# Kernel tuning notes

Hardware: AMD Instinct MI355X
Metric: run time of the kernel (lower is better)

The kernel has to match this reference:

```python
import jax, jax.numpy as jnp
import numpy as np

B, NB, T, NC = 32, 55, 512, 8
D, H, E, K, DEPTH, FF = 128, 8, 8, 2, 4, 512  # embed, heads, experts, top_k, depth, ffn hidden=4*D
IN = NB * NC  # 440


def _ln(x, g, b, eps=1e-5):
    m = jnp.mean(x, axis=-1, keepdims=True)
    v = jnp.mean((x - m) ** 2, axis=-1, keepdims=True)
    return (x - m) / jnp.sqrt(v + eps) * g + b


def setup_inputs() -> dict:
    key = jax.random.key(0)
    ks = jax.random.split(key, 16)
    s = 0.02
    return {
        "x": jax.random.normal(ks[0], (B, NB, T, NC), jnp.float32),
        "proj_W": jax.random.normal(ks[1], (IN, D), jnp.float32) * s,
        "proj_b": jnp.zeros((D,), jnp.float32),
        "pos_embed": jax.random.normal(ks[2], (1, T, D), jnp.float32) * s,
        "ln1_g": jnp.ones((DEPTH, D), jnp.float32),
        "ln1_b": jnp.zeros((DEPTH, D), jnp.float32),
        "qkv_W": jax.random.normal(ks[3], (DEPTH, D, 3 * D), jnp.float32) * s,
        "qkv_b": jnp.zeros((DEPTH, 3 * D), jnp.float32),
        "out_W": jax.random.normal(ks[4], (DEPTH, D, D), jnp.float32) * s,
        "out_b": jnp.zeros((DEPTH, D), jnp.float32),
        "ln2_g": jnp.ones((DEPTH, D), jnp.float32),
        "ln2_b": jnp.zeros((DEPTH, D), jnp.float32),
        "gate_W": jax.random.normal(ks[5], (DEPTH, D, E), jnp.float32) * s,
        "w1": jax.random.normal(ks[6], (DEPTH, E, D, FF), jnp.float32) * s,
        "b1": jnp.zeros((DEPTH, E, FF), jnp.float32),
        "w2": jax.random.normal(ks[7], (DEPTH, E, FF, D), jnp.float32) * s,
        "b2": jnp.zeros((DEPTH, E, D), jnp.float32),
        "head_ln_g": jnp.ones((D,), jnp.float32),
        "head_ln_b": jnp.zeros((D,), jnp.float32),
        "head_W": jax.random.normal(ks[8], (D, 2), jnp.float32) * s,
        "head_b": jnp.zeros((2,), jnp.float32),
    }


def reference(x, proj_W, proj_b, pos_embed, ln1_g, ln1_b, qkv_W, qkv_b, out_W,
              out_b, ln2_g, ln2_b, gate_W, w1, b1, w2, b2, head_ln_g,
              head_ln_b, head_W, head_b):
    b, nb, t, nc = x.shape
    h = jnp.transpose(x, (0, 2, 1, 3)).reshape(b, t, nb * nc)  # [b,t,440]
    h = h @ proj_W + proj_b + pos_embed[:, :t, :]
    aux_total = jnp.float32(0.0)
    for i in range(DEPTH):
        # --- pre-LN multi-head self-attention ---
        z = _ln(h, ln1_g[i], ln1_b[i])
        qkv = z @ qkv_W[i] + qkv_b[i]
        q, k, v = jnp.split(qkv, 3, axis=-1)
        dh = D // H
        q = q.reshape(b, t, H, dh)
        k = k.reshape(b, t, H, dh)
        v = v.reshape(b, t, H, dh)
        att = jnp.einsum('bqhd,bkhd->bhqk', q, k) / jnp.sqrt(jnp.float32(dh))
        att = jax.nn.softmax(att, axis=-1)
        o = jnp.einsum('bhqk,bkhd->bqhd', att, v).reshape(b, t, D)
        h = h + o @ out_W[i] + out_b[i]
        # --- pre-LN top-k MoE FFN ---
        z = _ln(h, ln2_g[i], ln2_b[i])
        probs = jax.nn.softmax(z @ gate_W[i], axis=-1)  # [b,t,E]
        topv, topi = jax.lax.top_k(probs, K)
        wts = topv / jnp.sum(topv, axis=-1, keepdims=True)
        combine = jnp.sum(jax.nn.one_hot(topi, E, dtype=probs.dtype) * wts[..., None], axis=-2)  # [b,t,E]
        hid = jax.nn.gelu(jnp.einsum('btd,edf->btef', z, w1[i]) + b1[i])
        yexp = jnp.einsum('btef,efd->bted', hid, w2[i]) + b2[i]
        h = h + jnp.einsum('bte,bted->btd', combine, yexp)
        # Switch-style load-balancing auxiliary loss
        importance = probs.mean(axis=(0, 1))            # mean router prob per expert
        load = (combine > 0).astype(probs.dtype).mean(axis=(0, 1))  # dispatch fraction
        aux_total = aux_total + E * jnp.sum(importance * load)
    pooled = h.mean(axis=1)
    pooled = _ln(pooled, head_ln_g, head_ln_b)
    return pooled @ head_W + head_b, aux_total
```

## Files before the change

### kernel.cpp

```cpp
#include <hip/hip_runtime.h>
#include <hip/hip_bf16.h>
#include <cstdint>
#include <cstddef>

#define BT        16384
#define MAXASSIGN 33792
#define QSCALE    0.36067376022224085f

typedef __attribute__((ext_vector_type(8)))  short short8;
typedef __attribute__((ext_vector_type(4)))  short short4v;
typedef __attribute__((ext_vector_type(4)))  float f32x4;
typedef __attribute__((ext_vector_type(16))) float f32x16;

typedef const uint32_t __attribute__((address_space(1))) gas_u32;
typedef uint32_t __attribute__((address_space(3))) las_u32;

__device__ __forceinline__ void gload16(const void* g, void* l) {
    __builtin_amdgcn_global_load_lds((gas_u32*)g, (las_u32*)l, 16, 0, 0);
}

__device__ __forceinline__ float gelu_f(float x) {
    float u2l = (x + 0.044715f * x * x * x) * 2.3022081927f;
    float e = exp2f(u2l);
    float r = __builtin_amdgcn_rcpf(e + 1.0f);
    return x * e * r;
}

__device__ __forceinline__ unsigned pkbf(float a, float b) {
    __hip_bfloat16 ha = __float2bfloat16(a);
    __hip_bfloat16 hb = __float2bfloat16(b);
    unsigned short ua = *reinterpret_cast<unsigned short*>(&ha);
    unsigned short ub = *reinterpret_cast<unsigned short*>(&hb);
    return (unsigned)ua | ((unsigned)ub << 16);
}

__device__ __forceinline__ float bf2f(unsigned short u) {
    unsigned v = (unsigned)u << 16;
    return __uint_as_float(v);
}

__global__ __launch_bounds__(256) void transpose_kernel(const float* __restrict__ x,
                                                        __hip_bfloat16* __restrict__ xtb,
                                                        const float* __restrict__ projW,
                                                        __hip_bfloat16* __restrict__ projWt,
                                                        float* __restrict__ auxp,
                                                        float* __restrict__ impc,
                                                        unsigned* __restrict__ zrow) {
    __shared__ unsigned tile[64][228];
    const int tid = threadIdx.x;
    if (blockIdx.x == 480) {
        if (tid == 0) auxp[0] = 0.f;
        for (int u = tid; u < 4096; u += 256) impc[u] = 0.f;
        if (tid < 64) zrow[tid] = 0u;
        return;
    }
    if (blockIdx.x >= 256) {
        int idx = (blockIdx.x - 256) * 256 + tid;
        int k = idx % 448, n = idx / 448;
        projWt[idx] = __float2bfloat16(k < 440 ? projW[k * 128 + n] : 0.f);
        return;
    }
    const int b  = blockIdx.x >> 3;
    const int t0 = (blockIdx.x & 7) * 64;
    tile[tid >> 2][220 + (tid & 3)] = 0u;
    const int tt  = tid >> 2;
    const int ncp = tid & 3;
    for (int nb = 0; nb < 55; ++nb) {
        const float2* src = (const float2*)(x + (((size_t)(b * 55 + nb)) * 512 + t0) * 8);
        float2 v = src[tid];
        tile[tt][nb * 4 + ncp] = pkbf(v.x, v.y);
    }
    __syncthreads();
#pragma unroll
    for (int u = 0; u < 14; ++u) {
        int idx = u * 256 + tid;
        int t = idx / 56, c = idx % 56;
        *(uint4*)(xtb + ((size_t)b * 512 + t0 + t) * 448 + c * 8) =
            *(const uint4*)&tile[t][c * 4];
    }
}

__global__ __launch_bounds__(256) void wconvt4_kernel(
    const float* __restrict__ qkvW, __hip_bfloat16* __restrict__ qkvWt_,
    const float* __restrict__ outW, __hip_bfloat16* __restrict__ outWt_,
    const float* __restrict__ w1i, __hip_bfloat16* __restrict__ w1o,
    const float* __restrict__ w2i, __hip_bfloat16* __restrict__ w2o)
{
    __shared__ float tile[64][65];
    const int bid = blockIdx.x;
    const float* in; __hip_bfloat16* out; int K, N, blk;
    if (bid < 48)       { in = qkvW; out = qkvWt_; K = 128; N = 384; blk = bid; }
    else if (bid < 64)  { in = outW; out = outWt_; K = 128; N = 128; blk = bid - 48; }
    else if (bid < 576) { in = w1i;  out = w1o;    K = 128; N = 512; blk = bid - 64; }
    else                { in = w2i;  out = w2o;    K = 512; N = 128; blk = bid - 576; }
    const int kt = K >> 6, nt = N >> 6;
    const int per = kt * nt;
    const int bb  = blk / per;
    const int rem = blk % per;
    const int k0  = (rem / nt) << 6;
    const int n0  = (rem % nt) << 6;
    const int tid = threadIdx.x;

    const float* src = in + ((size_t)bb * K + k0) * N + n0;
    int tk = tid >> 4;
    int tn = (tid & 15) * 4;
#pragma unroll
    for (int r = 0; r < 4; ++r) {
        float4 v = *(const float4*)(src + (size_t)(tk + r * 16) * N + tn);
        tile[tk + r * 16][tn]     = v.x;
        tile[tk + r * 16][tn + 1] = v.y;
        tile[tk + r * 16][tn + 2] = v.z;
        tile[tk + r * 16][tn + 3] = v.w;
    }
    __syncthreads();
    int on = tid >> 2;
    int ok = (tid & 3) * 16;
    unsigned pk[8];
#pragma unroll
    for (int u = 0; u < 8; ++u)
        pk[u] = pkbf(tile[ok + 2 * u][on], tile[ok + 2 * u + 1][on]);
    uint4* dst = (uint4*)(out + ((size_t)bb * N + n0 + on) * K + k0 + ok);
    dst[0] = (uint4){pk[0], pk[1], pk[2], pk[3]};
    dst[1] = (uint4){pk[4], pk[5], pk[6], pk[7]};
}

template<int MODE, int BM>
__global__ __launch_bounds__(256) void mm_kernel(
    const __hip_bfloat16* __restrict__ A, const __hip_bfloat16* __restrict__ Wt,
    const float* __restrict__ bias, const float* __restrict__ extra,
    void* __restrict__ Cout, int K, int N)
{
    constexpr int FI = BM / 32;
    __shared__ short smem[16384];
    short* As = smem;
    short* Bs = smem + BM * 64;
    const int tid  = threadIdx.x;
    const int row0 = blockIdx.x * BM;
    const int col0 = blockIdx.y * 128;

    const int wave = tid >> 6, lane = tid & 63;
    const int crow = tid >> 3;
    const int cc   = tid & 7;

    f32x4 acc[FI][4];
#pragma unroll
    for (int i = 0; i < FI; ++i)
#pragma unroll
        for (int j = 0; j < 4; ++j) acc[i][j] = (f32x4){0.f, 0.f, 0.f, 0.f};

    const int wm = (wave >> 1) * (BM / 2), wn = (wave & 1) * 64;
    const int lr = lane & 15, q = lane >> 4;

    for (int k0 = 0; k0 < K; k0 += 64) {
#pragma unroll
        for (int p = 0; p < FI; ++p) {
            int row = p * 32 + crow;
            int sc  = (cc ^ (row & 7)) << 3;
            short* la = &As[(p * 32 + wave * 8) * 64];
            gload16(A + (size_t)(row0 + row) * K + k0 + sc, la);
        }
#pragma unroll
        for (int p = 0; p < 4; ++p) {
            int row = p * 32 + crow;
            int sc  = (cc ^ (row & 7)) << 3;
            short* lb = &Bs[(p * 32 + wave * 8) * 64];
            gload16(Wt + (size_t)(col0 + row) * K + k0 + sc, lb);
        }
        __syncthreads();
#pragma unroll
        for (int s = 0; s < 2; ++s) {
            short8 af[FI], bf[4];
#pragma unroll
            for (int f = 0; f < FI; ++f) {
                int m = wm + f * 16 + lr;
                af[f] = *(const short8*)&As[(m * 8 + ((s * 4 + q) ^ (m & 7))) * 8];
            }
#pragma unroll
            for (int f = 0; f < 4; ++f) {
                int n = wn + f * 16 + lr;
                bf[f] = *(const short8*)&Bs[(n * 8 + ((s * 4 + q) ^ (n & 7))) * 8];
            }
#pragma unroll
            for (int i = 0; i < FI; ++i)
#pragma unroll
                for (int j = 0; j < 4; ++j)
                    acc[i][j] = __builtin_amdgcn_mfma_f32_16x16x32_bf16(
                        bf[j], af[i], acc[i][j], 0, 0, 0);
        }
        __syncthreads();
    }

    float4 b4[4];
#pragma unroll
    for (int j = 0; j < 4; ++j)
        b4[j] = *(const float4*)&bias[col0 + wn + j * 16 + q * 4];

    if constexpr (MODE == 5) {
        const bool qsc = (col0 == 0);
#pragma unroll
        for (int i = 0; i < FI; ++i) {
            int trow = wm + i * 16 + lr;
#pragma unroll
            for (int j = 0; j < 4; ++j) {
                int cb = wn + j * 16 + q * 4;
                float v0 = acc[i][j][0] + b4[j].x;
                float v1 = acc[i][j][1] + b4[j].y;
                float v2 = acc[i][j][2] + b4[j].z;
                float v3 = acc[i][j][3] + b4[j].w;
                if (qsc) { v0 *= QSCALE; v1 *= QSCALE; v2 *= QSCALE; v3 *= QSCALE; }
                uint2 pk = {pkbf(v0, v1), pkbf(v2, v3)};
                int ch = cb >> 3;
                *(uint2*)((char*)smem + trow * 256 + ((ch ^ (trow & 7)) << 4)
                          + ((cb & 7) << 1)) = pk;
            }
        }
        __syncthreads();
        __hip_bfloat16* outb = (__hip_bfloat16*)Cout;
        constexpr int TPR = 256 / BM;
        constexpr int CPT = 16 / TPR;
        int rrow = tid / TPR;
        size_t pbase = (size_t)(col0 >> 7) * 8 * BT * 16;
#pragma unroll
        for (int u = 0; u < CPT; ++u) {
            int c = (tid % TPR) * CPT + u;
            uint4 d = *(const uint4*)((char*)smem + rrow * 256
                                      + ((c ^ (rrow & 7)) << 4));
            size_t dst = pbase + ((size_t)(c >> 1) * BT + row0 + rrow) * 16
                       + (c & 1) * 8;
            *(uint4*)(outb + dst) = d;
        }
    } else {
        float* outf = (float*)Cout;
#pragma unroll
        for (int i = 0; i < FI; ++i) {
            int trow = wm + i * 16 + lr;
#pragma unroll
            for (int j = 0; j < 4; ++j) {
                int cb = wn + j * 16 + q * 4;
                f32x4 v = acc[i][j];
                v[0] += b4[j].x; v[1] += b4[j].y;
                v[2] += b4[j].z; v[3] += b4[j].w;
                int ch = cb >> 2;
                *(f32x4*)((char*)smem + trow * 512
                          + ((ch ^ (trow & 7)) << 4)) = v;
            }
        }
        __syncthreads();
        {
            int rrow = tid >> 2;
            int grow = row0 + rrow;
            size_t rb = (size_t)grow * N + col0;
#pragma unroll
            for (int u = 0; u < 8; ++u) {
                int c = (tid & 3) * 8 + u;
                f32x4 d = *(const f32x4*)((char*)smem + rrow * 512
                                          + ((c ^ (rrow & 7)) << 4));
                int gcol = col0 + c * 4;
                if constexpr (MODE == 0) {
                    float4 p = *(const float4*)&extra[(grow & 511) * 128 + gcol];
                    d[0] += p.x; d[1] += p.y; d[2] += p.z; d[3] += p.w;
                } else if constexpr (MODE == 2) {
                    float4 p = *(const float4*)&extra[rb + c * 4];
                    d[0] += p.x; d[1] += p.y; d[2] += p.z; d[3] += p.w;
                }
                *(f32x4*)&outf[rb + c * 4] = d;
            }
        }
        __syncthreads();
    }
}

__global__ __launch_bounds__(256) void moe_kernel(
    const __hip_bfloat16* __restrict__ zbf, const __hip_bfloat16* __restrict__ w1t,
    const float* __restrict__ b1, const __hip_bfloat16* __restrict__ w2t,
    const float* __restrict__ b2, __hip_bfloat16* __restrict__ yout,
    const int* __restrict__ moff, const int* __restrict__ atok,
    const float* __restrict__ awt)
{
    __shared__ short smem[24576];
    short* zA = smem;
    short* Bs = smem + 8192;
    short* hA = smem + 16384;
    const int tid  = threadIdx.x;
    const int row0 = blockIdx.x * 64;
    if (row0 >= moff[8]) return;
    int e = 0;
    while (moff[e + 1] <= row0) ++e;
    const __hip_bfloat16* W1 = w1t + (size_t)e * 512 * 128;
    const __hip_bfloat16* W2 = w2t + (size_t)e * 128 * 512;
    const float* bb1 = b1 + e * 512;
    const float* bb2 = b2 + e * 128;
    const int lim = moff[e] + moff[9 + e];

    const int wave = tid >> 6, lane = tid & 63;
    const int crow = tid >> 3;
    const int cc   = tid & 7;

    int srow[2];
#pragma unroll
    for (int p = 0; p < 2; ++p) {
        int grow = row0 + p * 32 + crow;
        srow[p] = (grow < lim) ? atok[grow] : BT;
    }

#pragma unroll
    for (int ks = 0; ks < 2; ++ks)
#pragma unroll
        for (int p = 0; p < 2; ++p) {
            int row = p * 32 + crow;
            int sc  = (cc ^ (row & 7)) << 3;
            gload16(zbf + (size_t)srow[p] * 128 + ks * 64 + sc,
                    &zA[ks * 4096 + (p * 32 + wave * 8) * 64]);
        }

    const int wm = (wave >> 1) * 32, wn = (wave & 1) * 64;
    const int lr = lane & 15, q = lane >> 4;

    f32x4 acc2[2][4];
#pragma unroll
    for (int i = 0; i < 2; ++i)
#pragma unroll
        for (int j = 0; j < 4; ++j) acc2[i][j] = (f32x4){0.f, 0.f, 0.f, 0.f};

    __syncthreads();

    for (int f0 = 0; f0 < 4; ++f0) {
        f32x4 acc1[2][4];
#pragma unroll
        for (int i = 0; i < 2; ++i)
#pragma unroll
            for (int j = 0; j < 4; ++j) acc1[i][j] = (f32x4){0.f, 0.f, 0.f, 0.f};

#pragma unroll
        for (int ks = 0; ks < 2; ++ks) {
#pragma unroll
            for (int p = 0; p < 4; ++p) {
                int row = p * 32 + crow;
                int sc  = (cc ^ (row & 7)) << 3;
                gload16(W1 + (size_t)(f0 * 128 + row) * 128 + ks * 64 + sc,
                        &Bs[(p * 32 + wave * 8) * 64]);
            }
            __syncthreads();
#pragma unroll
            for (int s = 0; s < 2; ++s) {
                short8 af[2], bf[4];
#pragma unroll
                for (int f = 0; f < 2; ++f) {
                    int m = wm + f * 16 + lr;
                    af[f] = *(const short8*)&zA[ks * 4096
                            + (m * 8 + ((s * 4 + q) ^ (m & 7))) * 8];
                }
#pragma unroll
                for (int f = 0; f < 4; ++f) {
                    int n = wn + f * 16 + lr;
                    bf[f] = *(const short8*)&Bs[(n * 8 + ((s * 4 + q) ^ (n & 7))) * 8];
                }
#pragma unroll
                for (int i = 0; i < 2; ++i)
#pragma unroll
                    for (int j = 0; j < 4; ++j)
                        acc1[i][j] = __builtin_amdgcn_mfma_f32_16x16x32_bf16(
                            bf[j], af[i], acc1[i][j], 0, 0, 0);
            }
            __syncthreads();
        }

#pragma unroll
        for (int i = 0; i < 2; ++i) {
            int trow = wm + i * 16 + lr;
#pragma unroll
            for (int j = 0; j < 4; ++j) {
                int cb = wn + j * 16 + q * 4;
                float4 g4 = *(const float4*)&bb1[f0 * 128 + cb];
                float v0 = gelu_f(acc1[i][j][0] + g4.x);
                float v1 = gelu_f(acc1[i][j][1] + g4.y);
                float v2 = gelu_f(acc1[i][j][2] + g4.z);
                float v3 = gelu_f(acc1[i][j][3] + g4.w);
                uint2 pk = {pkbf(v0, v1), pkbf(v2, v3)};
                int s2 = cb >> 6, kl = cb & 63, ch = kl >> 3;
                *(uint2*)((char*)hA + s2 * 8192 + trow * 128
                          + ((ch ^ (trow & 7)) << 4) + ((kl & 7) << 1)) = pk;
            }
        }
        __syncthreads();

#pragma unroll
        for (int ks2 = 0; ks2 < 2; ++ks2) {
#pragma unroll
            for (int p = 0; p < 4; ++p) {
                int row = p * 32 + crow;
                int sc  = (cc ^ (row & 7)) << 3;
                gload16(W2 + (size_t)row * 512 + f0 * 128 + ks2 * 64 + sc,
                        &Bs[(p * 32 + wave * 8) * 64]);
            }
            __syncthreads();
#pragma unroll
            for (int s = 0; s < 2; ++s) {
                short8 af[2], bf[4];
#pragma unroll
                for (int f = 0; f < 2; ++f) {
                    int m = wm + f * 16 + lr;
                    af[f] = *(const short8*)&hA[ks2 * 4096
                            + (m * 8 + ((s * 4 + q) ^ (m & 7))) * 8];
                }
#pragma unroll
                for (int f = 0; f < 4; ++f) {
                    int n = wn + f * 16 + lr;
                    bf[f] = *(const short8*)&Bs[(n * 8 + ((s * 4 + q) ^ (n & 7))) * 8];
                }
#pragma unroll
                for (int i = 0; i < 2; ++i)
#pragma unroll
                    for (int j = 0; j < 4; ++j)
                        acc2[i][j] = __builtin_amdgcn_mfma_f32_16x16x32_bf16(
                            bf[j], af[i], acc2[i][j], 0, 0, 0);
            }
            __syncthreads();
        }
    }

    float4 b4[4];
#pragma unroll
    for (int j = 0; j < 4; ++j)
        b4[j] = *(const float4*)&bb2[wn + j * 16 + q * 4];
#pragma unroll
    for (int i = 0; i < 2; ++i) {
        int trow = wm + i * 16 + lr;
        float aw = awt[row0 + trow];
#pragma unroll
        for (int j = 0; j < 4; ++j) {
            int cb = wn + j * 16 + q * 4;
            float v0 = (acc2[i][j][0] + b4[j].x) * aw;
            float v1 = (acc2[i][j][1] + b4[j].y) * aw;
            float v2 = (acc2[i][j][2] + b4[j].z) * aw;
            float v3 = (acc2[i][j][3] + b4[j].w) * aw;
            uint2 pk = {pkbf(v0, v1), pkbf(v2, v3)};
            int ch = cb >> 3;
            *(uint2*)((char*)Bs + trow * 256 + ((ch ^ (trow & 7)) << 4)
                      + ((cb & 7) << 1)) = pk;
        }
    }
    __syncthreads();
    {
        int rrow = tid >> 2;
        size_t rb = (size_t)(row0 + rrow) * 128;
#pragma unroll
        for (int u = 0; u < 4; ++u) {
            int c = (tid & 3) * 4 + u;
            uint4 d = *(const uint4*)((char*)Bs + rrow * 256
                                      + ((c ^ (rrow & 7)) << 4));
            *(uint4*)(yout + rb + c * 8) = d;
        }
    }
}

__global__ __launch_bounds__(256) void ln_kernel(const float* __restrict__ x,
                                                 const float* __restrict__ g,
                                                 const float* __restrict__ b,
                                                 __hip_bfloat16* __restrict__ zbf) {
    int wave = threadIdx.x >> 6, lane = threadIdx.x & 63;
    size_t row = (size_t)blockIdx.x * 4 + wave;
    const float* xr = x + row * 128;
    float a0 = xr[lane], a1 = xr[lane + 64];
    float s = a0 + a1;
#pragma unroll
    for (int off = 32; off > 0; off >>= 1) s += __shfl_xor(s, off);
    float mean = s * (1.f / 128.f);
    float d0 = a0 - mean, d1 = a1 - mean;
    float v = d0 * d0 + d1 * d1;
#pragma unroll
    for (int off = 32; off > 0; off >>= 1) v += __shfl_xor(v, off);
    float inv = rsqrtf(v * (1.f / 128.f) + 1e-5f);
    zbf[row * 128 + lane]      = __float2bfloat16(d0 * inv * g[lane] + b[lane]);
    zbf[row * 128 + lane + 64] = __float2bfloat16(d1 * inv * g[lane + 64] + b[lane + 64]);
}

__global__ __launch_bounds__(1024) void attn_kernel(const __hip_bfloat16* __restrict__ qkv,
                                                    __hip_bfloat16* __restrict__ o) {
    __shared__ short Ks[512 * 24];
    __shared__ short Vt[17 * 520];
    const int hh = blockIdx.x, b = blockIdx.y;
    const int tid = threadIdx.x;
    const __hip_bfloat16* Qh = qkv + ((size_t)(0 * 8 + hh) * BT + b * 512) * 16;
    const __hip_bfloat16* Kh = qkv + ((size_t)(1 * 8 + hh) * BT + b * 512) * 16;
    const __hip_bfloat16* Vh = qkv + ((size_t)(2 * 8 + hh) * BT + b * 512) * 16;

    if (tid < 512) {
        int r = tid;
        const uint4* ksrc = (const uint4*)(Kh + (size_t)r * 16);
        uint4 k0 = ksrc[0], k1 = ksrc[1];
        *(uint4*)&Ks[r * 24 + 0] = k0;
        *(uint4*)&Ks[r * 24 + 8] = k1;
    } else {
        int r = tid - 512;
        const uint4* vsrc = (const uint4*)(Vh + (size_t)r * 16);
        uint4 v0 = vsrc[0], v1 = vsrc[1];
        unsigned vv[8] = {v0.x, v0.y, v0.z, v0.w, v1.x, v1.y, v1.z, v1.w};
#pragma unroll
        for (int c = 0; c < 8; ++c) {
            Vt[(2 * c)     * 520 + r] = (short)(vv[c] & 0xffff);
            Vt[(2 * c + 1) * 520 + r] = (short)(vv[c] >> 16);
        }
        Vt[16 * 520 + r] = (short)0x3F80;
    }
    __syncthreads();

    const int wave = tid >> 6, lane = tid & 63;
    const int lm = lane & 31, lh = lane >> 5;
    const int qrow0 = wave * 32;

    short8 qf = *(const short8*)(Qh + (size_t)(qrow0 + lm) * 16 + lh * 8);

    f32x16 accO;
#pragma unroll
    for (int r = 0; r < 16; ++r) accO[r] = 0.f;

    for (int kc = 0; kc < 16; ++kc) {
        short8 kf = *(const short8*)&Ks[(kc * 32 + lm) * 24 + lh * 8];
        int vr = (lm < 16) ? lm : 16;
        const short* vb2 = &Vt[vr * 520 + kc * 32];
        short4v va  = *(const short4v*)(vb2 + 4 * lh);
        short4v vbq = *(const short4v*)(vb2 + 8 + 4 * lh);
        short4v vc  = *(const short4v*)(vb2 + 16 + 4 * lh);
        short4v vd  = *(const short4v*)(vb2 + 24 + 4 * lh);
        short8 vf0, vf1;
#pragma unroll
        for (int j = 0; j < 4; ++j) {
            vf0[j] = va[j];  vf0[4 + j] = vbq[j];
            vf1[j] = vc[j];  vf1[4 + j] = vd[j];
        }
        f32x16 st;
#pragma unroll
        for (int r = 0; r < 16; ++r) st[r] = 0.f;
        st = __builtin_amdgcn_mfma_f32_32x32x16_bf16(kf, qf, st, 0, 0, 0);
        short8 pf0, pf1;
#pragma unroll
        for (int r = 0; r < 8; ++r) {
            pf0[r] = (short)(__float_as_uint(exp2f(st[r]))     >> 16);
            pf1[r] = (short)(__float_as_uint(exp2f(st[8 + r])) >> 16);
        }
        accO = __builtin_amdgcn_mfma_f32_32x32x16_bf16(pf0, vf0, accO, 0, 0, 0);
        accO = __builtin_amdgcn_mfma_f32_32x32x16_bf16(pf1, vf1, accO, 0, 0, 0);
    }

    __syncthreads();
#pragma unroll
    for (int r = 0; r < 16; ++r) {
        float val = accO[r];
        float s = __shfl(val, (lane & 32) + 16);
        if (lm < 16) {
            int qr = qrow0 + (r & 3) + 8 * (r >> 2) + 4 * lh;
            __hip_bfloat16 hv = __float2bfloat16(val / s);
            Ks[qr * 16 + lm] = *reinterpret_cast<short*>(&hv);
        }
    }
    __syncthreads();
    {
        int rr = tid >> 1;
        int hf = tid & 1;
        uint4 d = *(const uint4*)&Ks[rr * 16 + hf * 8];
        *(uint4*)(o + ((size_t)b * 512 + rr) * 128 + hh * 16 + hf * 8) = d;
    }
}

__global__ __launch_bounds__(256) void ln2gate_kernel(
    const float* __restrict__ x, const float* __restrict__ g, const float* __restrict__ b,
    const float* __restrict__ gW, __hip_bfloat16* __restrict__ zbf,
    int* __restrict__ topi, float* __restrict__ topw,
    float* __restrict__ impS, int* __restrict__ cntS)
{
    __shared__ float simp[8];
    __shared__ int scnt[8];
    const int tid = threadIdx.x;
    if (tid < 8) { simp[tid] = 0.f; scnt[tid] = 0; }
    __syncthreads();
    const int wave = tid >> 6, lane = tid & 63;
    const size_t row = (size_t)blockIdx.x * 4 + wave;
    const float* xr = x + row * 128;
    float a0 = xr[lane], a1 = xr[lane + 64];
    float s = a0 + a1;
#pragma unroll
    for (int off = 32; off > 0; off >>= 1) s += __shfl_xor(s, off);
    float mean = s * (1.f / 128.f);
    float d0 = a0 - mean, d1 = a1 - mean;
    float v = d0 * d0 + d1 * d1;
#pragma unroll
    for (int off = 32; off > 0; off >>= 1) v += __shfl_xor(v, off);
    float inv = rsqrtf(v * (1.f / 128.f) + 1e-5f);
    float o0 = d0 * inv * g[lane] + b[lane];
    float o1 = d1 * inv * g[lane + 64] + b[lane + 64];
    zbf[row * 128 + lane]      = __float2bfloat16(o0);
    zbf[row * 128 + lane + 64] = __float2bfloat16(o1);
    float4 gA = *(const float4*)&gW[lane * 8];
    float4 gB = *(const float4*)&gW[lane * 8 + 4];
    float4 gC = *(const float4*)&gW[(lane + 64) * 8];
    float4 gD = *(const float4*)&gW[(lane + 64) * 8 + 4];
    float lg[8];
    lg[0] = o0 * gA.x + o1 * gC.x;  lg[1] = o0 * gA.y + o1 * gC.y;
    lg[2] = o0 * gA.z + o1 * gC.z;  lg[3] = o0 * gA.w + o1 * gC.w;
    lg[4] = o0 * gB.x + o1 * gD.x;  lg[5] = o0 * gB.y + o1 * gD.y;
    lg[6] = o0 * gB.z + o1 * gD.z;  lg[7] = o0 * gB.w + o1 * gD.w;
#pragma unroll
    for (int e = 0; e < 8; ++e)
#pragma unroll
        for (int off = 32; off > 0; off >>= 1) lg[e] += __shfl_xor(lg[e], off);
    if (lane == 0) {
        float p[8];
        float mx = lg[0];
#pragma unroll
        for (int k = 1; k < 8; ++k) mx = fmaxf(mx, lg[k]);
        float ssum = 0.f;
#pragma unroll
        for (int k = 0; k < 8; ++k) { p[k] = expf(lg[k] - mx); ssum += p[k]; }
        float pinv = 1.f / ssum;
#pragma unroll
        for (int k = 0; k < 8; ++k) p[k] *= pinv;
        int i0 = 0; float v0 = p[0];
#pragma unroll
        for (int k = 1; k < 8; ++k) if (p[k] > v0) { v0 = p[k]; i0 = k; }
        int i1 = -1; float v1 = -1.f;
#pragma unroll
        for (int k = 0; k < 8; ++k) if (k != i0 && p[k] > v1) { v1 = p[k]; i1 = k; }
        float wsum = v0 + v1;
        topi[row * 2] = i0;  topi[row * 2 + 1] = i1;
        topw[row * 2] = v0 / wsum;  topw[row * 2 + 1] = v1 / wsum;
#pragma unroll
        for (int k = 0; k < 8; ++k) atomicAdd(&simp[k], p[k]);
        atomicAdd(&scnt[i0], 1); atomicAdd(&scnt[i1], 1);
    }
    __syncthreads();
    if (tid < 8) {
        int slot = (blockIdx.x >> 6) * 8 + tid;
        atomicAdd(&impS[slot], simp[tid]);
        atomicAdd(&cntS[slot], scnt[tid]);
    }
}

__global__ __launch_bounds__(256) void scatter_kernel(
    const int* __restrict__ topi, const float* __restrict__ topw,
    const int* __restrict__ cntS, const float* __restrict__ impS,
    int* __restrict__ atok, float* __restrict__ awt, int* __restrict__ tokpos,
    int* __restrict__ moffw, float* __restrict__ aux)
{
    __shared__ int lcnt[8];
    __shared__ int lbase[8];
    __shared__ int csum[8];
    __shared__ float isum[8];
    const int tid = threadIdx.x;
    const int blk = blockIdx.x;
    if (tid < 64) {
        int e = tid & 7, grp = tid >> 3;
        int ct = 0, cp = 0; float im = 0.f;
        for (int g = 0; g < 8; ++g) {
            int sl = grp * 8 + g;
            int vv = cntS[sl * 8 + e];
            ct += vv;
            cp += (sl < blk) ? vv : 0;
            im += impS[sl * 8 + e];
        }
#pragma unroll
        for (int off = 32; off >= 8; off >>= 1) {
            ct += __shfl_down(ct, off);
            cp += __shfl_down(cp, off);
            im += __shfl_down(im, off);
        }
        if (tid < 8) { csum[tid] = ct; isum[tid] = im; lbase[tid] = cp; lcnt[tid] = 0; }
    }
    __syncthreads();
    if (tid < 8) {
        int t = 0;
        for (int k = 0; k < tid; ++k) t += (csum[k] + 127) & ~127;
        lbase[tid] += t;
    }
    if (blk == 0 && tid == 64) {
        int t = 0; float s = 0.f;
        for (int k = 0; k < 8; ++k) {
            int ck = csum[k];
            moffw[k] = t;
            moffw[9 + k] = ck;
            t += (ck + 127) & ~127;
            s += (isum[k] * (1.f / 16384.f)) * ((float)ck * (1.f / 16384.f));
        }
        moffw[8] = t;
        aux[0] += 8.f * s;
    }
    __syncthreads();
    const int token = blk * 256 + tid;
    const int e0 = topi[token * 2], e1 = topi[token * 2 + 1];
    const float w0 = topw[token * 2], w1 = topw[token * 2 + 1];
    const int l0 = atomicAdd(&lcnt[e0], 1);
    const int l1 = atomicAdd(&lcnt[e1], 1);
    const int p0 = lbase[e0] + l0;
    const int p1 = lbase[e1] + l1;
    atok[p0] = token;  awt[p0] = w0;  tokpos[token * 2]     = p0;
    atok[p1] = token;  awt[p1] = w1;  tokpos[token * 2 + 1] = p1;
}

__global__ __launch_bounds__(256) void combine_ln_kernel(
    const __hip_bfloat16* __restrict__ yw, const int* __restrict__ tokpos,
    float* __restrict__ h, const float* __restrict__ g, const float* __restrict__ b,
    __hip_bfloat16* __restrict__ zbf)
{
    const int tid = threadIdx.x;
    const int wave = tid >> 6, lane = tid & 63;
    const size_t row = (size_t)blockIdx.x * 4 + wave;
    const int p0 = tokpos[row * 2], p1 = tokpos[row * 2 + 1];
    const unsigned short* y0 = (const unsigned short*)(yw + (size_t)p0 * 128);
    const unsigned short* y1 = (const unsigned short*)(yw + (size_t)p1 * 128);
    float a0 = h[row * 128 + lane]      + bf2f(y0[lane])      + bf2f(y1[lane]);
    float a1 = h[row * 128 + lane + 64] + bf2f(y0[lane + 64]) + bf2f(y1[lane + 64]);
    h[row * 128 + lane]      = a0;
    h[row * 128 + lane + 64] = a1;
    if (zbf) {
        float s = a0 + a1;
#pragma unroll
        for (int off = 32; off > 0; off >>= 1) s += __shfl_xor(s, off);
        float mean = s * (1.f / 128.f);
        float d0 = a0 - mean, d1 = a1 - mean;
        float v = d0 * d0 + d1 * d1;
#pragma unroll
        for (int off = 32; off > 0; off >>= 1) v += __shfl_xor(v, off);
        float inv = rsqrtf(v * (1.f / 128.f) + 1e-5f);
        zbf[row * 128 + lane]      = __float2bfloat16(d0 * inv * g[lane] + b[lane]);
        zbf[row * 128 + lane + 64] = __float2bfloat16(d1 * inv * g[lane + 64] + b[lane + 64]);
    }
}

__global__ __launch_bounds__(1024) void head_kernel(const float* __restrict__ h,
                                                    const float* __restrict__ g,
                                                    const float* __restrict__ bb,
                                                    const float* __restrict__ hW,
                                                    const float* __restrict__ hb,
                                                    const float* __restrict__ aux,
                                                    float* __restrict__ out) {
    __shared__ float part[8][128];
    __shared__ float red[128];
    __shared__ float pl[128];
    int b = blockIdx.x, tid = threadIdx.x;
    int c = tid & 127, w = tid >> 7;
    float s = 0.f;
    for (int t = w; t < 512; t += 8) s += h[((size_t)b * 512 + t) * 128 + c];
    part[w][c] = s;
    __syncthreads();
    float pooled = 0.f;
    if (tid < 128) {
#pragma unroll
        for (int k = 0; k < 8; ++k) pooled += part[k][tid];
        pooled *= (1.f / 512.f);
        red[tid] = pooled;
    }
    __syncthreads();
    for (int st = 64; st > 0; st >>= 1) { if (tid < st) red[tid] += red[tid + st]; __syncthreads(); }
    float mean = red[0] * (1.f / 128.f);
    __syncthreads();
    float d = pooled - mean;
    if (tid < 128) red[tid] = d * d;
    __syncthreads();
    for (int st = 64; st > 0; st >>= 1) { if (tid < st) red[tid] += red[tid + st]; __syncthreads(); }
    float var = red[0] * (1.f / 128.f);
    if (tid < 128) pl[tid] = d / sqrtf(var + 1e-5f) * g[tid] + bb[tid];
    __syncthreads();
    if (tid < 2) {
        float acc = hb[tid];
        for (int k = 0; k < 128; ++k) acc += pl[k] * hW[k * 2 + tid];
        out[b * 2 + tid] = acc;
    }
    if (b == 0 && tid == 0) out[64] = aux[0];
}

extern "C" void kernel_launch(void* const* d_in, const int* in_sizes, int n_in,
                              void* d_out, int out_size, void* d_ws, size_t ws_size,
                              hipStream_t stream) {
    (void)in_sizes; (void)n_in; (void)out_size; (void)ws_size;
    const float* x      = (const float*)d_in[0];
    const float* proj_W = (const float*)d_in[1];
    const float* proj_b = (const float*)d_in[2];
    const float* pos    = (const float*)d_in[3];
    const float* ln1_g  = (const float*)d_in[4];
    const float* ln1_b  = (const float*)d_in[5];
    const float* qkv_W  = (const float*)d_in[6];
    const float* qkv_b  = (const float*)d_in[7];
    const float* out_W  = (const float*)d_in[8];
    const float* out_b  = (const float*)d_in[9];
    const float* ln2_g  = (const float*)d_in[10];
    const float* ln2_b  = (const float*)d_in[11];
    const float* gate_W = (const float*)d_in[12];
    const float* w1     = (const float*)d_in[13];
    const float* b1     = (const float*)d_in[14];
    const float* w2     = (const float*)d_in[15];
    const float* b2     = (const float*)d_in[16];
    const float* hl_g   = (const float*)d_in[17];
    const float* hl_b   = (const float*)d_in[18];
    const float* head_W = (const float*)d_in[19];
    const float* head_b = (const float*)d_in[20];
    float* outp = (float*)d_out;

    float* ws = (float*)d_ws;
    size_t off = 0;
    auto alloc = [&](size_t n) { float* p = ws + off; off += (n + 63) & ~(size_t)63; return p; };
    float* xtb_f   = alloc((size_t)BT * 224);
    float* h       = alloc((size_t)BT * 128);
    float* zbf_f   = alloc((size_t)(BT + 1) * 64);
    float* qkvbf_f = alloc((size_t)BT * 192);
    float* obbf_f  = alloc((size_t)BT * 64);
    float* yw      = alloc((size_t)MAXASSIGN * 64);
    float* projWt_f= alloc(128 * 448 / 2);
    float* qkvWt_f = alloc(4 * 384 * 128 / 2);
    float* outWt_f = alloc(4 * 128 * 128 / 2);
    float* w1t_f   = alloc((size_t)32 * 512 * 128 / 2);
    float* w2t_f   = alloc((size_t)32 * 128 * 512 / 2);
    float* topw    = alloc(32768);
    float* awt     = alloc(MAXASSIGN);
    float* impc    = alloc(4096);
    float* auxp    = alloc(1);
    int* topi      = (int*)alloc(32768);
    int* atok      = (int*)alloc(MAXASSIGN);
    int* tokpos    = (int*)alloc(32768);
    int* moff      = (int*)alloc(32);

    __hip_bfloat16* xtb    = (__hip_bfloat16*)xtb_f;
    __hip_bfloat16* zbf    = (__hip_bfloat16*)zbf_f;
    __hip_bfloat16* qkvbf  = (__hip_bfloat16*)qkvbf_f;
    __hip_bfloat16* obbf   = (__hip_bfloat16*)obbf_f;
    __hip_bfloat16* ywb    = (__hip_bfloat16*)yw;
    __hip_bfloat16* projWt = (__hip_bfloat16*)projWt_f;
    __hip_bfloat16* qkvWt  = (__hip_bfloat16*)qkvWt_f;
    __hip_bfloat16* outWt  = (__hip_bfloat16*)outWt_f;
    __hip_bfloat16* w1t    = (__hip_bfloat16*)w1t_f;
    __hip_bfloat16* w2t    = (__hip_bfloat16*)w2t_f;

    transpose_kernel<<<481, 256, 0, stream>>>(
        x, xtb, proj_W, projWt, auxp, impc,
        (unsigned*)((char*)zbf + (size_t)BT * 256));
    wconvt4_kernel<<<1088, 256, 0, stream>>>(qkv_W, qkvWt, out_W, outWt,
                                             w1, w1t, w2, w2t);

    mm_kernel<0, 64><<<dim3(256, 1), 256, 0, stream>>>(
        xtb, projWt, proj_b, pos, h, 448, 128);
    ln_kernel<<<4096, 256, 0, stream>>>(h, ln1_g, ln1_b, zbf);

    for (int i = 0; i < 4; ++i) {
        float* impS = impc + (size_t)i * 1024;
        int*   cntS = (int*)(impc + (size_t)i * 1024 + 512);
        mm_kernel<5, 64><<<dim3(256, 3), 256, 0, stream>>>(
            zbf, qkvWt + (size_t)i * 384 * 128, qkv_b + i * 384, nullptr, qkvbf,
            128, 384);
        attn_kernel<<<dim3(8, 32), 1024, 0, stream>>>(qkvbf, obbf);
        mm_kernel<2, 64><<<dim3(256, 1), 256, 0, stream>>>(
            obbf, outWt + (size_t)i * 128 * 128, out_b + i * 128, h, h,
            128, 128);
        ln2gate_kernel<<<4096, 256, 0, stream>>>(h, ln2_g + i * 128, ln2_b + i * 128,
                                                 gate_W + (size_t)i * 128 * 8, zbf,
                                                 topi, topw, impS, cntS);
        scatter_kernel<<<64, 256, 0, stream>>>(topi, topw, cntS, impS,
                                               atok, awt, tokpos, moff, auxp);
        moe_kernel<<<528, 256, 0, stream>>>(
            zbf, w1t + (size_t)i * 8 * 512 * 128, b1 + (size_t)i * 8 * 512,
            w2t + (size_t)i * 8 * 128 * 512, b2 + (size_t)i * 8 * 128,
            ywb, moff, atok, awt);
        combine_ln_kernel<<<4096, 256, 0, stream>>>(ywb, tokpos, h,
                                                    ln1_g + (i + 1 < 4 ? (i + 1) * 128 : 0),
                                                    ln1_b + (i + 1 < 4 ? (i + 1) * 128 : 0),
                                                    (i < 3) ? zbf : (__hip_bfloat16*)nullptr);
    }
    head_kernel<<<32, 1024, 0, stream>>>(h, hl_g, hl_b, head_W, head_b, auxp, outp);
}
```

Baseline: 560.6 us.

## Fuse MoE combine into expert kernel via atomic adds into residual

The MoE expert kernel now scatters its weighted outputs straight into the fp32 residual h with per-element float atomicAdds, replacing the bf16 staging buffer and the separate combine+LN kernel. A plain LN kernel then recomputes zbf for the next layer. This removes a global round trip of expert outputs and the tokpos bookkeeping. In exchange it issues many scalar atomics with uncoalesced per-row access, and the order of floating-point summation becomes nondeterministic.

```diff
diff --git a/kernel.cpp b/kernel.cpp
--- a/kernel.cpp
+++ b/kernel.cpp
@@ -273,7 +273,7 @@
 __global__ __launch_bounds__(256) void moe_kernel(
     const __hip_bfloat16* __restrict__ zbf, const __hip_bfloat16* __restrict__ w1t,
     const float* __restrict__ b1, const __hip_bfloat16* __restrict__ w2t,
-    const float* __restrict__ b2, __hip_bfloat16* __restrict__ yout,
+    const float* __restrict__ b2, float* __restrict__ h,
     const int* __restrict__ moff, const int* __restrict__ atok,
     const float* __restrict__ awt)
 {
@@ -425,31 +425,19 @@
         b4[j] = *(const float4*)&bb2[wn + j * 16 + q * 4];
 #pragma unroll
     for (int i = 0; i < 2; ++i) {
-        int trow = wm + i * 16 + lr;
-        float aw = awt[row0 + trow];
-#pragma unroll
-        for (int j = 0; j < 4; ++j) {
-            int cb = wn + j * 16 + q * 4;
-            float v0 = (acc2[i][j][0] + b4[j].x) * aw;
-            float v1 = (acc2[i][j][1] + b4[j].y) * aw;
-            float v2 = (acc2[i][j][2] + b4[j].z) * aw;
-            float v3 = (acc2[i][j][3] + b4[j].w) * aw;
-            uint2 pk = {pkbf(v0, v1), pkbf(v2, v3)};
-            int ch = cb >> 3;
-            *(uint2*)((char*)Bs + trow * 256 + ((ch ^ (trow & 7)) << 4)
-                      + ((cb & 7) << 1)) = pk;
-        }
-    }
-    __syncthreads();
-    {
-        int rrow = tid >> 2;
-        size_t rb = (size_t)(row0 + rrow) * 128;
-#pragma unroll
-        for (int u = 0; u < 4; ++u) {
-            int c = (tid & 3) * 4 + u;
-            uint4 d = *(const uint4*)((char*)Bs + rrow * 256
-                                      + ((c ^ (rrow & 7)) << 4));
-            *(uint4*)(yout + rb + c * 8) = d;
+        int slot = row0 + wm + i * 16 + lr;
+        if (slot < lim) {
+            int token = atok[slot];
+            float aw = awt[slot];
+            float* hrow = h + (size_t)token * 128;
+#pragma unroll
+            for (int j = 0; j < 4; ++j) {
+                int cb = wn + j * 16 + q * 4;
+                atomicAdd(&hrow[cb + 0], (acc2[i][j][0] + b4[j].x) * aw);
+                atomicAdd(&hrow[cb + 1], (acc2[i][j][1] + b4[j].y) * aw);
+                atomicAdd(&hrow[cb + 2], (acc2[i][j][2] + b4[j].z) * aw);
+                atomicAdd(&hrow[cb + 3], (acc2[i][j][3] + b4[j].w) * aw);
+            }
         }
     }
 }
@@ -639,7 +627,7 @@
 __global__ __launch_bounds__(256) void scatter_kernel(
     const int* __restrict__ topi, const float* __restrict__ topw,
     const int* __restrict__ cntS, const float* __restrict__ impS,
-    int* __restrict__ atok, float* __restrict__ awt, int* __restrict__ tokpos,
+    int* __restrict__ atok, float* __restrict__ awt,
     int* __restrict__ moffw, float* __restrict__ aux)
 {
     __shared__ int lcnt[8];
@@ -692,38 +680,8 @@
     const int l1 = atomicAdd(&lcnt[e1], 1);
     const int p0 = lbase[e0] + l0;
     const int p1 = lbase[e1] + l1;
-    atok[p0] = token;  awt[p0] = w0;  tokpos[token * 2]     = p0;
-    atok[p1] = token;  awt[p1] = w1;  tokpos[token * 2 + 1] = p1;
-}
-
-__global__ __launch_bounds__(256) void combine_ln_kernel(
-    const __hip_bfloat16* __restrict__ yw, const int* __restrict__ tokpos,
-    float* __restrict__ h, const float* __restrict__ g, const float* __restrict__ b,
-    __hip_bfloat16* __restrict__ zbf)
-{
-    const int tid = threadIdx.x;
-    const int wave = tid >> 6, lane = tid & 63;
-    const size_t row = (size_t)blockIdx.x * 4 + wave;
-    const int p0 = tokpos[row * 2], p1 = tokpos[row * 2 + 1];
-    const unsigned short* y0 = (const unsigned short*)(yw + (size_t)p0 * 128);
-    const unsigned short* y1 = (const unsigned short*)(yw + (size_t)p1 * 128);
-    float a0 = h[row * 128 + lane]      + bf2f(y0[lane])      + bf2f(y1[lane]);
-    float a1 = h[row * 128 + lane + 64] + bf2f(y0[lane + 64]) + bf2f(y1[lane + 64]);
-    h[row * 128 + lane]      = a0;
-    h[row * 128 + lane + 64] = a1;
-    if (zbf) {
-        float s = a0 + a1;
-#pragma unroll
-        for (int off = 32; off > 0; off >>= 1) s += __shfl_xor(s, off);
-        float mean = s * (1.f / 128.f);
-        float d0 = a0 - mean, d1 = a1 - mean;
-        float v = d0 * d0 + d1 * d1;
-#pragma unroll
-        for (int off = 32; off > 0; off >>= 1) v += __shfl_xor(v, off);
-        float inv = rsqrtf(v * (1.f / 128.f) + 1e-5f);
-        zbf[row * 128 + lane]      = __float2bfloat16(d0 * inv * g[lane] + b[lane]);
-        zbf[row * 128 + lane + 64] = __float2bfloat16(d1 * inv * g[lane + 64] + b[lane + 64]);
-    }
+    atok[p0] = token;  awt[p0] = w0;
+    atok[p1] = token;  awt[p1] = w1;
 }
 
 __global__ __launch_bounds__(1024) void head_kernel(const float* __restrict__ h,
@@ -803,7 +761,6 @@
     float* zbf_f   = alloc((size_t)(BT + 1) * 64);
     float* qkvbf_f = alloc((size_t)BT * 192);
     float* obbf_f  = alloc((size_t)BT * 64);
-    float* yw      = alloc((size_t)MAXASSIGN * 64);
     float* projWt_f= alloc(128 * 448 / 2);
     float* qkvWt_f = alloc(4 * 384 * 128 / 2);
     float* outWt_f = alloc(4 * 128 * 128 / 2);
@@ -815,14 +772,12 @@
     float* auxp    = alloc(1);
     int* topi      = (int*)alloc(32768);
     int* atok      = (int*)alloc(MAXASSIGN);
-    int* tokpos    = (int*)alloc(32768);
     int* moff      = (int*)alloc(32);
 
     __hip_bfloat16* xtb    = (__hip_bfloat16*)xtb_f;
     __hip_bfloat16* zbf    = (__hip_bfloat16*)zbf_f;
     __hip_bfloat16* qkvbf  = (__hip_bfloat16*)qkvbf_f;
     __hip_bfloat16* obbf   = (__hip_bfloat16*)obbf_f;
-    __hip_bfloat16* ywb    = (__hip_bfloat16*)yw;
     __hip_bfloat16* projWt = (__hip_bfloat16*)projWt_f;
     __hip_bfloat16* qkvWt  = (__hip_bfloat16*)qkvWt_f;
     __hip_bfloat16* outWt  = (__hip_bfloat16*)outWt_f;
@@ -853,15 +808,14 @@
                                                  gate_W + (size_t)i * 128 * 8, zbf,
                                                  topi, topw, impS, cntS);
         scatter_kernel<<<64, 256, 0, stream>>>(topi, topw, cntS, impS,
-                                               atok, awt, tokpos, moff, auxp);
+                                               atok, awt, moff, auxp);
         moe_kernel<<<528, 256, 0, stream>>>(
             zbf, w1t + (size_t)i * 8 * 512 * 128, b1 + (size_t)i * 8 * 512,
             w2t + (size_t)i * 8 * 128 * 512, b2 + (size_t)i * 8 * 128,
-            ywb, moff, atok, awt);
-        combine_ln_kernel<<<4096, 256, 0, stream>>>(ywb, tokpos, h,
-                                                    ln1_g + (i + 1 < 4 ? (i + 1) * 128 : 0),
-                                                    ln1_b + (i + 1 < 4 ? (i + 1) * 128 : 0),
-                                                    (i < 3) ? zbf : (__hip_bfloat16*)nullptr);
+            h, moff, atok, awt);
+        if (i < 3)
+            ln_kernel<<<4096, 256, 0, stream>>>(h, ln1_g + (i + 1) * 128,
+                                                ln1_b + (i + 1) * 128, zbf);
     }
     head_kernel<<<32, 1024, 0, stream>>>(h, hl_g, hl_b, head_W, head_b, auxp, outp);
 }
```

New measurement: 750.8 us. 1.34x slower.
